# Performance work log

Hardware: AMD Instinct MI355X
Metric: run time of the kernel (lower is better)

## Reference

```python
import jax, jax.numpy as jnp
import numpy as np

NUM_EMBEDDINGS = 8192
EMBEDDING_DIM = 256
COMMITMENT_COST = 0.25


def setup_inputs() -> dict:
    key = jax.random.key(0)
    k1, k2 = jax.random.split(key)
    inputs = jax.random.normal(k1, (16, 2048, EMBEDDING_DIM), dtype=jnp.float32)
    # codebook initialized uniform(-1/K, 1/K) as in the torch module
    codebook = jax.random.uniform(
        k2, (NUM_EMBEDDINGS, EMBEDDING_DIM), dtype=jnp.float32,
        minval=-1.0 / NUM_EMBEDDINGS, maxval=1.0 / NUM_EMBEDDINGS)
    return {"inputs": inputs, "codebook": codebook}


def reference(inputs, codebook):
    B, T, D = inputs.shape
    flat = inputs.reshape(-1, D)                      # [BT, D]
    distances = (
        jnp.sum(flat * flat, axis=1, keepdims=True)
        + jnp.sum(codebook * codebook, axis=1)
        - 2.0 * jnp.matmul(flat, codebook.T)
    )
    idx = jnp.argmin(distances, axis=1)               # [BT]
    quantized = codebook[idx].reshape(B, T, D)        # gather == one-hot @ codebook
    e_latent_loss = jnp.mean((jax.lax.stop_gradient(quantized) - inputs) ** 2)
    q_latent_loss = jnp.mean((quantized - jax.lax.stop_gradient(inputs)) ** 2)
    loss = q_latent_loss + COMMITMENT_COST * e_latent_loss
    # straight-through estimator
    quantized_st = inputs + jax.lax.stop_gradient(quantized - inputs)
    return quantized_st, idx.reshape(B, T), loss
```

## Files before the change

### kernel.cpp

```cpp
#include <hip/hip_runtime.h>
#include <hip/hip_bf16.h>
#include <stdint.h>

#define D      256
#define K      8192
#define NROWS  32768
#define QELEMS 8388608

typedef __attribute__((ext_vector_type(8))) short bf16x8;
typedef __attribute__((ext_vector_type(4))) float f32x4;
typedef unsigned int u32;
typedef unsigned short u16;

__device__ __forceinline__ u16 f2bf(float f) {
    u32 b = __float_as_uint(f);
    return (u16)((b + 0x7fffu + ((b >> 16) & 1u)) >> 16);
}

__global__ __launch_bounds__(256) void vq_prep_kernel(
    const float* __restrict__ cb, u16* __restrict__ ch,
    float* __restrict__ se, float* __restrict__ loss_sum) {
    int row = blockIdx.x * 4 + (threadIdx.x >> 6);
    int l = threadIdx.x & 63;
    float4 v = *(const float4*)(cb + (size_t)row * D + l * 4);
    ushort4 o;
    o.x = f2bf(v.x); o.y = f2bf(v.y); o.z = f2bf(v.z); o.w = f2bf(v.w);
    *(ushort4*)(ch + (size_t)row * D + l * 4) = o;
    float s = v.x * v.x + v.y * v.y + v.z * v.z + v.w * v.w;
    #pragma unroll
    for (int off = 32; off > 0; off >>= 1) s += __shfl_down(s, off, 64);
    if (l == 0) se[row] = s;
    if (blockIdx.x == 0 && threadIdx.x == 0) *loss_sum = 0.f;
}

__global__ __launch_bounds__(256, 2) void vq_filter_kernel(
    const u16* __restrict__ ch, const float* __restrict__ x,
    const float* __restrict__ se, u32* __restrict__ cand)
{
    __shared__ __align__(16) u16 As[2][16384];

    const int tid  = threadIdx.x;
    const int lane = tid & 63;
    const int wave = tid >> 6;
    const int l15  = lane & 15;
    const int l4   = lane >> 4;
    const int row0 = blockIdx.x * 64;

    bf16x8 Bf[4][8];
    #pragma unroll
    for (int nt = 0; nt < 4; ++nt) {
        const float* xr = x + (size_t)(row0 + nt * 16 + l15) * D + l4 * 8;
        #pragma unroll
        for (int c = 0; c < 8; ++c) {
            float4 a = *(const float4*)(xr + c * 32);
            float4 b = *(const float4*)(xr + c * 32 + 4);
            bf16x8 f;
            f[0] = (short)f2bf(a.x); f[1] = (short)f2bf(a.y);
            f[2] = (short)f2bf(a.z); f[3] = (short)f2bf(a.w);
            f[4] = (short)f2bf(b.x); f[5] = (short)f2bf(b.y);
            f[6] = (short)f2bf(b.z); f[7] = (short)f2bf(b.w);
            Bf[nt][c] = f;
        }
    }

    float b0[4], b1[4]; int c0[4], c1[4];
    #pragma unroll
    for (int nt = 0; nt < 4; ++nt) { b0[nt] = 1e30f; b1[nt] = 1e30f; c0[nt] = 0; c1[nt] = 0; }

    #pragma unroll
    for (int i = 0; i < 8; ++i) {
        int g = wave * 8 + i;
        const u16* gp = ch + (size_t)((g & 3) * 16 + l15) * D + (g >> 2) * 32 + l4 * 8;
        u16* lb = &As[0][(size_t)g * 512];
        __builtin_amdgcn_global_load_lds(
            (const __attribute__((address_space(1))) u32*)gp,
            (__attribute__((address_space(3))) u32*)lb, 16, 0, 0);
    }
    __syncthreads();

    int buf = 0;
    #pragma unroll 1
    for (int ct = 0; ct < 128; ++ct) {
        const int k0 = ct << 6;

        if (ct + 1 < 128) {
            const int kn = (ct + 1) << 6;
            #pragma unroll
            for (int i = 0; i < 8; ++i) {
                int g = wave * 8 + i;
                const u16* gp = ch + (size_t)(kn + (g & 3) * 16 + l15) * D + (g >> 2) * 32 + l4 * 8;
                u16* lb = &As[buf ^ 1][(size_t)g * 512];
                __builtin_amdgcn_global_load_lds(
                    (const __attribute__((address_space(1))) u32*)gp,
                    (__attribute__((address_space(3))) u32*)lb, 16, 0, 0);
            }
        }

        const u16* cb_t = &As[buf][0];
        f32x4 acc[4];
        #pragma unroll
        for (int nt = 0; nt < 4; ++nt) acc[nt] = (f32x4){0.f, 0.f, 0.f, 0.f};

        #pragma unroll
        for (int c = 0; c < 8; ++c) {
            bf16x8 Af = *(const bf16x8*)(cb_t + (size_t)((c * 4 + wave) * 64 + lane) * 8);
            acc[0] = __builtin_amdgcn_mfma_f32_16x16x32_bf16(Af, Bf[0][c], acc[0], 0, 0, 0);
            acc[1] = __builtin_amdgcn_mfma_f32_16x16x32_bf16(Af, Bf[1][c], acc[1], 0, 0, 0);
            acc[2] = __builtin_amdgcn_mfma_f32_16x16x32_bf16(Af, Bf[2][c], acc[2], 0, 0, 0);
            acc[3] = __builtin_amdgcn_mfma_f32_16x16x32_bf16(Af, Bf[3][c], acc[3], 0, 0, 0);
        }

        f32x4 sev = *(const f32x4*)(se + k0 + wave * 16 + l4 * 4);

        #pragma unroll
        for (int nt = 0; nt < 4; ++nt) {
            float t0 = fmaf(-2.f, acc[nt][0], sev[0]);
            float t1 = fmaf(-2.f, acc[nt][1], sev[1]);
            float t2 = fmaf(-2.f, acc[nt][2], sev[2]);
            float t3 = fmaf(-2.f, acc[nt][3], sev[3]);
            float tmn = fminf(fminf(t0, t1), fminf(t2, t3));
            if (tmn < b1[nt]) {
                #pragma unroll
                for (int r = 0; r < 4; ++r) {
                    float t = fmaf(-2.f, acc[nt][r], sev[r]);
                    int  cv = k0 + wave * 16 + l4 * 4 + r;
                    bool in0 = t < b0[nt];
                    bool in1 = t < b1[nt];
                    float ob0 = b0[nt]; int oc0 = c0[nt];
                    b1[nt] = in0 ? ob0 : (in1 ? t  : b1[nt]);
                    c1[nt] = in0 ? oc0 : (in1 ? cv : c1[nt]);
                    b0[nt] = in0 ? t  : ob0;
                    c0[nt] = in0 ? cv : oc0;
                }
            }
        }

        __syncthreads();
        buf ^= 1;
    }

    float* Mv = (float*)&As[0][0];
    u32*   Mc = (u32*)(Mv + 64 * 33);
    #pragma unroll
    for (int nt = 0; nt < 4; ++nt) {
        int rl = nt * 16 + l15;
        int g  = wave * 4 + l4;
        Mv[rl * 33 + g * 2]     = b0[nt];
        Mv[rl * 33 + g * 2 + 1] = b1[nt];
        Mc[rl * 33 + g * 2]     = (u32)c0[nt];
        Mc[rl * 33 + g * 2 + 1] = (u32)c1[nt];
    }
    __syncthreads();

    for (int tsk = tid; tsk < 512; tsk += 256) {
        int row = tsk >> 3, m = tsk & 7;
        const float* v  = Mv + row * 33 + m * 4;
        const u32*   cc = Mc + row * 33 + m * 4;
        float v00 = v[0],  v01 = v[1],  v10 = v[2],  v11 = v[3];
        u32   c00 = cc[0], c01 = cc[1], c10 = cc[2], c11 = cc[3];
        bool  aw  = v00 <= v10;
        u32   w0c = aw ? c00 : c10;
        float s1  = aw ? v10 : v00; u32 s1c = aw ? c10 : c00;
        float s2  = aw ? v01 : v11; u32 s2c = aw ? c01 : c11;
        u32   w1c = (s2 <= s1) ? s2c : s1c;
        cand[(size_t)(row0 + row) * 16 + m * 2]     = w0c;
        cand[(size_t)(row0 + row) * 16 + m * 2 + 1] = w1c;
    }
}

__global__ __launch_bounds__(1024) void vq_rescore_kernel(
    const float* __restrict__ x, const float* __restrict__ cb,
    const float* __restrict__ se, const u32* __restrict__ cand,
    float* __restrict__ out, float* __restrict__ loss_sum)
{
    const int wave = threadIdx.x >> 6;
    const int lane = threadIdx.x & 63;
    const int row  = blockIdx.x * 16 + wave;

    float4 xv = *(const float4*)(x + (size_t)row * D + lane * 4);
    float sx = xv.x * xv.x + xv.y * xv.y + xv.z * xv.z + xv.w * xv.w;
    #pragma unroll
    for (int o = 1; o < 64; o <<= 1) sx += __shfl_xor(sx, o, 64);

    u32 myc = cand[(size_t)row * 16 + (lane & 15)];
    float best = 1e30f; int bk = 0x7fffffff;
    #pragma unroll 4
    for (int j = 0; j < 16; ++j) {
        int code = __shfl((int)myc, j, 64);
        float4 ev = *(const float4*)(cb + (size_t)code * D + lane * 4);
        float p = xv.x * ev.x + xv.y * ev.y + xv.z * ev.z + xv.w * ev.w;
        #pragma unroll
        for (int o = 1; o < 64; o <<= 1) p += __shfl_xor(p, o, 64);
        float dist = (sx + se[code]) - 2.0f * p;
        if (dist < best || (dist == best && code < bk)) { best = dist; bk = code; }
    }

    float4 q = *(const float4*)(cb + (size_t)bk * D + lane * 4);
    *(float4*)(out + (size_t)row * D + lane * 4) = q;
    float dx = q.x - xv.x, dy = q.y - xv.y, dz = q.z - xv.z, dw = q.w - xv.w;
    float s = dx * dx + dy * dy + dz * dz + dw * dw;
    #pragma unroll
    for (int o = 1; o < 64; o <<= 1) s += __shfl_xor(s, o, 64);
    if (lane == 0) out[QELEMS + row] = (float)bk;

    __shared__ float red[16];
    if (lane == 0) red[wave] = s;
    __syncthreads();
    if (threadIdx.x == 0) {
        float t = 0.f;
        #pragma unroll
        for (int w2 = 0; w2 < 16; ++w2) t += red[w2];
        atomicAdd(loss_sum, t);
    }
}

__global__ void vq_fin_kernel(const float* __restrict__ loss_sum, float* __restrict__ out) {
    out[QELEMS + NROWS] = 1.25f * (*loss_sum) * (1.0f / (float)QELEMS);
}

extern "C" void kernel_launch(void* const* d_in, const int* in_sizes, int n_in,
                              void* d_out, int out_size, void* d_ws, size_t ws_size,
                              hipStream_t stream) {
    const float* x  = (const float*)d_in[0];
    const float* cb = (const float*)d_in[1];
    float* out = (float*)d_out;

    u16* ch = (u16*)d_out;

    char* ws = (char*)d_ws;
    float* loss_sum = (float*)ws;
    float* sebuf    = (float*)(ws + 4096);
    u32*   cand     = (u32*)(ws + 65536);

    vq_prep_kernel<<<K / 4, 256, 0, stream>>>(cb, ch, sebuf, loss_sum);
    vq_filter_kernel<<<NROWS / 64, 256, 0, stream>>>(ch, x, sebuf, cand);
    vq_rescore_kernel<<<NROWS / 16, 1024, 0, stream>>>(x, cb, sebuf, cand, out, loss_sum);
    vq_fin_kernel<<<1, 1, 0, stream>>>(loss_sum, out);
}
```

Baseline: 405.1 us.

## Load codebook fragments directly into registers instead of LDS double-buffering

Replaces the LDS double-buffered codebook staging (global_load_lds plus a __syncthreads per tile) with per-wave direct global loads of bf16 A-fragments into two register sets, software-pipelined across pairs of tiles. This removes block-wide barriers and LDS traffic. Since each wave reads a distinct 16-row slice, there is no intra-block sharing to lose. The cost is more VGPR pressure (two 8-fragment buffers) and reliance on L2/L1 caching of the codebook across blocks.

```diff
diff --git a/kernel.cpp b/kernel.cpp
--- a/kernel.cpp
+++ b/kernel.cpp
@@ -37,7 +37,8 @@
     const u16* __restrict__ ch, const float* __restrict__ x,
     const float* __restrict__ se, u32* __restrict__ cand)
 {
-    __shared__ __align__(16) u16 As[2][16384];
+    __shared__ float Mv[64 * 33];
+    __shared__ u32   Mc[64 * 33];
 
     const int tid  = threadIdx.x;
     const int lane = tid & 63;
@@ -67,80 +68,63 @@
     #pragma unroll
     for (int nt = 0; nt < 4; ++nt) { b0[nt] = 1e30f; b1[nt] = 1e30f; c0[nt] = 0; c1[nt] = 0; }
 
-    #pragma unroll
-    for (int i = 0; i < 8; ++i) {
-        int g = wave * 8 + i;
-        const u16* gp = ch + (size_t)((g & 3) * 16 + l15) * D + (g >> 2) * 32 + l4 * 8;
-        u16* lb = &As[0][(size_t)g * 512];
-        __builtin_amdgcn_global_load_lds(
-            (const __attribute__((address_space(1))) u32*)gp,
-            (__attribute__((address_space(3))) u32*)lb, 16, 0, 0);
-    }
-    __syncthreads();
-
-    int buf = 0;
+    const u16* apl = ch + (size_t)(wave * 16 + l15) * D + l4 * 8;
+
+#define LOAD_AF(AF, CT) do {                                                  \
+    const u16* _p = apl + (size_t)(CT) * 16384;                               \
+    _Pragma("unroll")                                                         \
+    for (int c = 0; c < 8; ++c) (AF)[c] = *(const bf16x8*)(_p + c * 32);      \
+} while (0)
+
+#define COMP_TILE(AF, CT) do {                                                \
+    const int k0 = (CT) << 6;                                                 \
+    f32x4 sev = *(const f32x4*)(se + k0 + wave * 16 + l4 * 4);                \
+    f32x4 acc[4];                                                             \
+    _Pragma("unroll")                                                         \
+    for (int nt = 0; nt < 4; ++nt) acc[nt] = (f32x4){0.f, 0.f, 0.f, 0.f};     \
+    _Pragma("unroll")                                                         \
+    for (int c = 0; c < 8; ++c) {                                             \
+        acc[0] = __builtin_amdgcn_mfma_f32_16x16x32_bf16((AF)[c], Bf[0][c], acc[0], 0, 0, 0); \
+        acc[1] = __builtin_amdgcn_mfma_f32_16x16x32_bf16((AF)[c], Bf[1][c], acc[1], 0, 0, 0); \
+        acc[2] = __builtin_amdgcn_mfma_f32_16x16x32_bf16((AF)[c], Bf[2][c], acc[2], 0, 0, 0); \
+        acc[3] = __builtin_amdgcn_mfma_f32_16x16x32_bf16((AF)[c], Bf[3][c], acc[3], 0, 0, 0); \
+    }                                                                         \
+    _Pragma("unroll")                                                         \
+    for (int nt = 0; nt < 4; ++nt) {                                          \
+        float t0 = fmaf(-2.f, acc[nt][0], sev[0]);                            \
+        float t1 = fmaf(-2.f, acc[nt][1], sev[1]);                            \
+        float t2 = fmaf(-2.f, acc[nt][2], sev[2]);                            \
+        float t3 = fmaf(-2.f, acc[nt][3], sev[3]);                            \
+        float tmn = fminf(fminf(t0, t1), fminf(t2, t3));                      \
+        if (tmn < b1[nt]) {                                                   \
+            _Pragma("unroll")                                                 \
+            for (int r = 0; r < 4; ++r) {                                     \
+                float t = fmaf(-2.f, acc[nt][r], sev[r]);                     \
+                int  cv = k0 + wave * 16 + l4 * 4 + r;                        \
+                bool in0 = t < b0[nt];                                        \
+                bool in1 = t < b1[nt];                                        \
+                float ob0 = b0[nt]; int oc0 = c0[nt];                         \
+                b1[nt] = in0 ? ob0 : (in1 ? t  : b1[nt]);                     \
+                c1[nt] = in0 ? oc0 : (in1 ? cv : c1[nt]);                     \
+                b0[nt] = in0 ? t  : ob0;                                      \
+                c0[nt] = in0 ? cv : oc0;                                      \
+            }                                                                 \
+        }                                                                     \
+    }                                                                         \
+} while (0)
+
+    bf16x8 AfA[8], AfB[8];
+    LOAD_AF(AfA, 0);
     #pragma unroll 1
-    for (int ct = 0; ct < 128; ++ct) {
-        const int k0 = ct << 6;
-
-        if (ct + 1 < 128) {
-            const int kn = (ct + 1) << 6;
-            #pragma unroll
-            for (int i = 0; i < 8; ++i) {
-                int g = wave * 8 + i;
-                const u16* gp = ch + (size_t)(kn + (g & 3) * 16 + l15) * D + (g >> 2) * 32 + l4 * 8;
-                u16* lb = &As[buf ^ 1][(size_t)g * 512];
-                __builtin_amdgcn_global_load_lds(
-                    (const __attribute__((address_space(1))) u32*)gp,
-                    (__attribute__((address_space(3))) u32*)lb, 16, 0, 0);
-            }
-        }
-
-        const u16* cb_t = &As[buf][0];
-        f32x4 acc[4];
-        #pragma unroll
-        for (int nt = 0; nt < 4; ++nt) acc[nt] = (f32x4){0.f, 0.f, 0.f, 0.f};
-
-        #pragma unroll
-        for (int c = 0; c < 8; ++c) {
-            bf16x8 Af = *(const bf16x8*)(cb_t + (size_t)((c * 4 + wave) * 64 + lane) * 8);
-            acc[0] = __builtin_amdgcn_mfma_f32_16x16x32_bf16(Af, Bf[0][c], acc[0], 0, 0, 0);
-            acc[1] = __builtin_amdgcn_mfma_f32_16x16x32_bf16(Af, Bf[1][c], acc[1], 0, 0, 0);
-            acc[2] = __builtin_amdgcn_mfma_f32_16x16x32_bf16(Af, Bf[2][c], acc[2], 0, 0, 0);
-            acc[3] = __builtin_amdgcn_mfma_f32_16x16x32_bf16(Af, Bf[3][c], acc[3], 0, 0, 0);
-        }
-
-        f32x4 sev = *(const f32x4*)(se + k0 + wave * 16 + l4 * 4);
-
-        #pragma unroll
-        for (int nt = 0; nt < 4; ++nt) {
-            float t0 = fmaf(-2.f, acc[nt][0], sev[0]);
-            float t1 = fmaf(-2.f, acc[nt][1], sev[1]);
-            float t2 = fmaf(-2.f, acc[nt][2], sev[2]);
-            float t3 = fmaf(-2.f, acc[nt][3], sev[3]);
-            float tmn = fminf(fminf(t0, t1), fminf(t2, t3));
-            if (tmn < b1[nt]) {
-                #pragma unroll
-                for (int r = 0; r < 4; ++r) {
-                    float t = fmaf(-2.f, acc[nt][r], sev[r]);
-                    int  cv = k0 + wave * 16 + l4 * 4 + r;
-                    bool in0 = t < b0[nt];
-                    bool in1 = t < b1[nt];
-                    float ob0 = b0[nt]; int oc0 = c0[nt];
-                    b1[nt] = in0 ? ob0 : (in1 ? t  : b1[nt]);
-                    c1[nt] = in0 ? oc0 : (in1 ? cv : c1[nt]);
-                    b0[nt] = in0 ? t  : ob0;
-                    c0[nt] = in0 ? cv : oc0;
-                }
-            }
-        }
-
-        __syncthreads();
-        buf ^= 1;
-    }
-
-    float* Mv = (float*)&As[0][0];
-    u32*   Mc = (u32*)(Mv + 64 * 33);
+    for (int ct = 0; ct < 128; ct += 2) {
+        LOAD_AF(AfB, ct + 1);
+        COMP_TILE(AfA, ct);
+        if (ct + 2 < 128) LOAD_AF(AfA, ct + 2);
+        COMP_TILE(AfB, ct + 1);
+    }
+#undef LOAD_AF
+#undef COMP_TILE
+
     #pragma unroll
     for (int nt = 0; nt < 4; ++nt) {
         int rl = nt * 16 + l15;
```

After: 405.1 us. About the same (-0.0%).
